# Kernel tuning notes

Hardware: AMD Instinct MI355X
Metric: run time of the kernel (lower is better)

Reference implementation:

```python
import jax, jax.numpy as jnp
import numpy as np

# Conv config (matches init_kwargs)
STRIDE = (1, 1)
PADDING = ((1, 1), (1, 1))
B, CIN, COUT, H, W = 16, 128, 256, 56, 56
KH, KW = 3, 3


def _conv(x, w):
    # NCHW input, OIHW kernel, zeros padding mode
    return jax.lax.conv_general_dilated(
        x, w, window_strides=STRIDE, padding=PADDING,
        dimension_numbers=("NCHW", "OIHW", "NCHW"))


def setup_inputs() -> dict:
    key = jax.random.key(0)
    ks = jax.random.split(key, 6)
    x = jax.random.normal(ks[0], (B, CIN, H, W), dtype=jnp.float32)
    # quantized weight: integer-valued floats (output of module.Q.quantize)
    weight = jnp.round(jax.random.normal(ks[1], (COUT, CIN, KH, KW), dtype=jnp.float32) * 4.0)
    act_s = jnp.asarray(0.0625, dtype=jnp.float32)   # exp2(log_act_s)
    act_q = jnp.asarray(16.0, dtype=jnp.float32)     # exp2(log_act_q)
    azp = jnp.asarray(-4.0, dtype=jnp.float32)       # rounded act zero point (scaled by guard_a)
    wzp = jnp.round(jax.random.normal(ks[2], (COUT,), dtype=jnp.float32) * 2.0)
    fp_scale = (jax.random.uniform(ks[3], (1, COUT, 1, 1), dtype=jnp.float32) + 0.5) * 1e-3
    # bias_full has spatial extent [1, COUT, H_out, W_out]
    bias = jax.random.normal(ks[4], (1, COUT, H, W), dtype=jnp.float32) * 0.1
    guard_a = jnp.asarray(2.0, dtype=jnp.float32)    # 2**act_guard_bit
    guard_w = jnp.asarray(2.0, dtype=jnp.float32)    # 2**weight_guard_bit
    return {"x": x, "weight": weight, "act_s": act_s, "act_q": act_q,
            "azp": azp, "wzp": wzp, "fp_scale": fp_scale, "bias": bias,
            "guard_a": guard_a, "guard_w": guard_w}


def reference(x, weight, act_s, act_q, azp, wzp, fp_scale, bias, guard_a, guard_w):
    # 1) Activation quantization: clamp to quant range then round to integer grid.
    zp = azp * act_s / guard_a
    xq = jnp.clip(x, zp, zp + act_q - act_s)
    xq = guard_a * jnp.round((xq - zp) / act_s)
    # 2) Main integer conv with quantized weights.
    c1 = _conv(xq, weight)
    # 3) Ones-kernel conv: output is identical across all COUT channels,
    #    so compute once as channel-sum followed by a single-channel box conv.
    s = jnp.sum(xq, axis=1, keepdims=True)  # [B, 1, H, W]
    ones_k = jnp.ones((1, 1) + weight.shape[2:], dtype=x.dtype)
    c2 = _conv(s, ones_k)  # [B, 1, H_out, W_out], broadcasts over channels
    # 4) Affine dequant + spatially-varying bias epilogue.
    out = guard_w * c1 + wzp[None, :, None, None] * c2
    return out * fp_scale + bias
```

## Files before the change

kernel.cpp:

```cpp
#include <hip/hip_runtime.h>

#define B_    16
#define CIN_  128
#define COUT_ 256
#define H_    56
#define W_    56
#define YP    58
#define XP    64

typedef int   i32x4 __attribute__((ext_vector_type(4)));
typedef float f4    __attribute__((ext_vector_type(4)));

#define AS_SZ 8192
#define BH_SZ 24704

__device__ __forceinline__ void gload16(const void* g, void* l) {
    __builtin_amdgcn_global_load_lds(
        (const __attribute__((address_space(1))) unsigned int*)g,
        (__attribute__((address_space(3))) unsigned int*)l,
        16, 0, 0);
}

__global__ __launch_bounds__(256) void k_prep(
    const float* __restrict__ x, const float* __restrict__ w,
    const float* __restrict__ p_act_s, const float* __restrict__ p_act_q,
    const float* __restrict__ p_azp,  const float* __restrict__ p_guard_a,
    signed char* __restrict__ xqU, signed char* __restrict__ wt,
    float* __restrict__ s_pad, float* __restrict__ Wsum)
{
    int t = threadIdx.x;
    int blk = blockIdx.x;

    if (blk < 928) {
        int b = blk / YP, y = blk - b * YP;
        __shared__ signed char shq[W_ * 144];
        signed char* orow = xqU + (size_t)blk * XP * CIN_;

        if (y == 0 || y == YP - 1) {
            i32x4 pv = {(int)0x80808080, (int)0x80808080,
                        (int)0x80808080, (int)0x80808080};
            *(i32x4*)(orow + t * 32)      = pv;
            *(i32x4*)(orow + t * 32 + 16) = pv;
            if (t < XP) s_pad[(size_t)blk * XP + t] = 0.0f;
            return;
        }
        int h = y - 1;
        float act_s = p_act_s[0], act_q = p_act_q[0];
        float azp = p_azp[0], ga = p_guard_a[0];
        float zp = azp * act_s / ga;
        float hi = zp + act_q - act_s;
        float inv_s = 1.0f / act_s;

        for (int i = 0; i < 28; ++i) {
            int e = i * 256 + t;
            int cin = e / 56;
            int ww = e - cin * 56;
            float v = x[(((size_t)b * CIN_ + cin) * H_ + h) * W_ + ww];
            v = fminf(fmaxf(v, zp), hi);
            float r = rintf((v - zp) * inv_s);
            float uq = rintf(ga * r * 0.5f) - 128.0f;
            shq[ww * 144 + cin] = (signed char)(int)uq;
        }
        __syncthreads();
        #pragma unroll
        for (int i = 0; i < 2; ++i) {
            int T = i * 256 + t;
            int xx = T >> 3;
            int c16 = T & 7;
            union { i32x4 v; signed char c[16]; } u;
            if (xx >= 1 && xx <= W_) {
                u.v = *(const i32x4*)(shq + (xx - 1) * 144 + c16 * 16);
            } else {
                u.v = (i32x4){(int)0x80808080, (int)0x80808080,
                              (int)0x80808080, (int)0x80808080};
            }
            *(i32x4*)(orow + (size_t)xx * CIN_ + c16 * 16) = u.v;
            int sum = 0;
            #pragma unroll
            for (int j = 0; j < 16; ++j) sum += (int)u.c[j];
            sum += __shfl_xor(sum, 1);
            sum += __shfl_xor(sum, 2);
            sum += __shfl_xor(sum, 4);
            if (c16 == 0)
                s_pad[(size_t)blk * XP + xx] = (float)(2 * sum + 32768);
        }
        return;
    }

    if (blk < 1216) {
        int o = ((blk - 928) * 256 + t) * 4;
        int tile = o >> 13;
        int m    = (o >> 6) & 127;
        int kk   = o & 63;
        int cb = tile & 1, cc = (tile >> 1) & 1, g = tile >> 2;
        int cout = cb * 128 + m;
        int cin0 = cc * 64 + kk;
        int dy = g / 3, dx = g - dy * 3;
        union { int v; signed char c[4]; } pk;
        #pragma unroll
        for (int j = 0; j < 4; ++j) {
            float v = w[(size_t)cout * 1152 + (cin0 + j) * 9 + dy * 3 + dx];
            pk.c[j] = (signed char)(int)v;
        }
        *(int*)(wt + o) = pk.v;
        return;
    }

    {
        int bw = blk - 1216;
        int cout = bw * 16 + (t >> 4);
        int part = t & 15;
        const float* base = w + (size_t)cout * 1152 + part * 72;
        float s = 0.f;
        for (int j = 0; j < 72; ++j) s += base[j];
        s += __shfl_xor(s, 1);
        s += __shfl_xor(s, 2);
        s += __shfl_xor(s, 4);
        s += __shfl_xor(s, 8);
        if (part == 0) Wsum[cout] = s;
        return;
    }
}

__global__ __launch_bounds__(256, 2) void k_gemm(
    const signed char* __restrict__ xqU,
    const signed char* __restrict__ wt,
    const float* __restrict__ s_pad,
    const float* __restrict__ Wsum,
    const float* __restrict__ wzp,
    const float* __restrict__ fps,
    const float* __restrict__ bias,
    const float* __restrict__ p_gw,
    float* __restrict__ out)
{
    __shared__ __align__(16) signed char As[2][AS_SZ];
    __shared__ __align__(16) signed char Bh[2][BH_SZ];
    __shared__ float c2s[4 * 56];

    int tid = threadIdx.x;
    int wv = tid >> 6, lane = tid & 63;
    int xl = lane & 15, q = lane >> 4;
    int p = blockIdx.x, cb = blockIdx.y;
    int b = p / 14, hp = p - b * 14;
    int h = hp * 4;
    int wm0 = (wv >> 1) * 64, wn0 = (wv & 1) * 128;

    if (tid < 224) {
        int rr = tid / 56, wp = tid - rr * 56;
        const float* sp = s_pad + ((size_t)(b * YP + h + rr)) * XP + wp;
        float a = 0.f;
        #pragma unroll
        for (int dy = 0; dy < 3; ++dy)
            #pragma unroll
            for (int dx = 0; dx < 3; ++dx)
                a += sp[dy * XP + dx];
        c2s[tid] = a;
    }

    i32x4 acc[4][8];
    #pragma unroll
    for (int mi = 0; mi < 4; ++mi)
        #pragma unroll
        for (int ni = 0; ni < 8; ++ni)
            acc[mi][ni] = (i32x4){0, 0, 0, 0};

    const signed char* xb = xqU + (size_t)(b * YP + h) * XP * CIN_;

    int a_base = (wm0 + xl) * 64 + q * 16;
    int bn_base[8];
    #pragma unroll
    for (int ni = 0; ni < 8; ++ni) {
        int n = wn0 + ni * 16 + xl;
        int rn = n >> 6, wp = n & 63;
        bn_base[ni] = (rn * XP + wp) * 64 + q * 16;
    }

    #define STAGE_A(buf_, g_, cc_)                                          \
        {                                                                   \
            const signed char* wsrc = wt + (size_t)((((g_)*2+(cc_))*2)+cb) * 8192; \
            signed char* dstb = As[buf_];                                   \
            _Pragma("unroll")                                               \
            for (int r_ = 0; r_ < 2; ++r_)                                  \
                gload16(wsrc + (r_ * 256 + tid) * 16,                       \
                        dstb + (r_ * 256 + wv * 64) * 16);                  \
        }
    #define STAGE_B(buf_, cc_)                                              \
        {                                                                   \
            signed char* dstb = Bh[buf_];                                   \
            _Pragma("unroll")                                               \
            for (int r_ = 0; r_ < 6; ++r_) {                                \
                int T_ = r_ * 256 + tid;                                    \
                int p_ = T_ & 3;                                            \
                int x_ = (T_ >> 2) & 63;                                    \
                int yy_ = T_ >> 8;                                          \
                gload16(xb + (size_t)(yy_ * XP + x_) * CIN_ + (cc_) * 64 + p_ * 16, \
                        dstb + (r_ * 256 + wv * 64) * 16);                  \
            }                                                               \
        }

    STAGE_A(0, 0, 0)
    STAGE_B(0, 0)
    __syncthreads();

    for (int i = 0; i < 18; ++i) {
        int cc = (i >= 9) ? 1 : 0;
        int g = i - cc * 9;
        if (i < 17) {
            int gn = g + 1, ccn = cc;
            if (gn == 9) { gn = 0; ccn = 1; }
            STAGE_A((i + 1) & 1, gn, ccn)
            if (gn == 0) STAGE_B(1, 1)
        }
        {
            const signed char* Ab = As[i & 1];
            const signed char* Bb = Bh[cc];
            int dy = g / 3, dx = g - dy * 3;
            int boff = dy * (XP * 64) + dx * 64;
            i32x4 af[4], bfr[8];
            #pragma unroll
            for (int mi = 0; mi < 4; ++mi)
                af[mi] = *(const i32x4*)(Ab + a_base + mi * 1024);
            #pragma unroll
            for (int ni = 0; ni < 8; ++ni)
                bfr[ni] = *(const i32x4*)(Bb + bn_base[ni] + boff);
            #pragma unroll
            for (int mi = 0; mi < 4; ++mi)
                #pragma unroll
                for (int ni = 0; ni < 8; ++ni)
                    acc[mi][ni] = __builtin_amdgcn_mfma_i32_16x16x64_i8(
                        af[mi], bfr[ni], acc[mi][ni], 0, 0, 0);
        }
        __syncthreads();
    }

    float gw = p_gw[0];
    #pragma unroll
    for (int mi = 0; mi < 4; ++mi) {
        #pragma unroll
        for (int r = 0; r < 4; ++r) {
            int cout = cb * 128 + wm0 + mi * 16 + q * 4 + r;
            float wz = wzp[cout], fs = fps[cout], ws = Wsum[cout];
            #pragma unroll
            for (int ni = 0; ni < 8; ++ni) {
                int n = wn0 + ni * 16 + xl;
                int wp = n & 63;
                if (wp < W_) {
                    int rn = n >> 6;
                    int hrow = h + rn;
                    float c1 = 2.0f * (float)acc[mi][ni][r] + 256.0f * ws;
                    float v = gw * c1 + wz * c2s[rn * 56 + wp];
                    out[(((size_t)b * COUT_ + cout) * H_ + hrow) * W_ + wp] =
                        v * fs + bias[((size_t)cout * H_ + hrow) * W_ + wp];
                }
            }
        }
    }
}

extern "C" void kernel_launch(void* const* d_in, const int* in_sizes, int n_in,
                              void* d_out, int out_size, void* d_ws, size_t ws_size,
                              hipStream_t stream)
{
    const float* x     = (const float*)d_in[0];
    const float* wht   = (const float*)d_in[1];
    const float* act_s = (const float*)d_in[2];
    const float* act_q = (const float*)d_in[3];
    const float* azp   = (const float*)d_in[4];
    const float* wzp   = (const float*)d_in[5];
    const float* fps   = (const float*)d_in[6];
    const float* bias  = (const float*)d_in[7];
    const float* ga    = (const float*)d_in[8];
    const float* gw    = (const float*)d_in[9];
    float* out = (float*)d_out;

    char* ws = (char*)d_ws;
    signed char* xqU  = (signed char*)(ws);
    signed char* wt   = (signed char*)(ws + 7602176);
    float*       spad = (float*)(ws + 7602176 + 294912);
    float*       Wsum = (float*)(ws + 7602176 + 294912 + 237568);

    k_prep<<<dim3(1232), dim3(256), 0, stream>>>(
        x, wht, act_s, act_q, azp, ga, xqU, wt, spad, Wsum);
    k_gemm<<<dim3(224, 2), dim3(256), 0, stream>>>(
        xqU, wt, spad, Wsum, wzp, fps, bias, gw, out);
}
```

Baseline: 143.9 us.

## Halve spatial tile, read weights directly from global, swizzle LDS input layout

Each block now covers 2 output rows instead of 4, so the grid doubles and per-wave accumulators shrink from 4x8 to 4x4 tiles. Weight tiles are no longer staged through LDS with double buffering; each wave loads A fragments straight from global/L2, which removes 16 of the 18 barriers. The input halo tile in LDS is XOR-swizzled across 16-byte slots to cut bank conflicts on B-fragment reads. The trade-off is more redundant halo loads and weight traffic from global memory, in exchange for lower register pressure and higher occupancy.

```diff
diff --git a/kernel.cpp b/kernel.cpp
--- a/kernel.cpp
+++ b/kernel.cpp
@@ -9,10 +9,8 @@
 #define XP    64
 
 typedef int   i32x4 __attribute__((ext_vector_type(4)));
-typedef float f4    __attribute__((ext_vector_type(4)));
-
-#define AS_SZ 8192
-#define BH_SZ 24704
+
+#define BH_SZ 16640
 
 __device__ __forceinline__ void gload16(const void* g, void* l) {
     __builtin_amdgcn_global_load_lds(
@@ -133,19 +131,19 @@
     const float* __restrict__ p_gw,
     float* __restrict__ out)
 {
-    __shared__ __align__(16) signed char As[2][AS_SZ];
     __shared__ __align__(16) signed char Bh[2][BH_SZ];
-    __shared__ float c2s[4 * 56];
+    __shared__ float c2s[2 * 56];
 
     int tid = threadIdx.x;
     int wv = tid >> 6, lane = tid & 63;
     int xl = lane & 15, q = lane >> 4;
     int p = blockIdx.x, cb = blockIdx.y;
-    int b = p / 14, hp = p - b * 14;
-    int h = hp * 4;
-    int wm0 = (wv >> 1) * 64, wn0 = (wv & 1) * 128;
-
-    if (tid < 224) {
+    int b = p / 28, hp = p - b * 28;
+    int h = hp * 2;
+    int wm0 = (wv >> 1) * 64;
+    int row = wv & 1;
+
+    if (tid < 112) {
         int rr = tid / 56, wp = tid - rr * 56;
         const float* sp = s_pad + ((size_t)(b * YP + h + rr)) * XP + wp;
         float a = 0.f;
@@ -157,100 +155,87 @@
         c2s[tid] = a;
     }
 
-    i32x4 acc[4][8];
-    #pragma unroll
-    for (int mi = 0; mi < 4; ++mi)
-        #pragma unroll
-        for (int ni = 0; ni < 8; ++ni)
-            acc[mi][ni] = (i32x4){0, 0, 0, 0};
-
     const signed char* xb = xqU + (size_t)(b * YP + h) * XP * CIN_;
 
-    int a_base = (wm0 + xl) * 64 + q * 16;
-    int bn_base[8];
-    #pragma unroll
-    for (int ni = 0; ni < 8; ++ni) {
-        int n = wn0 + ni * 16 + xl;
-        int rn = n >> 6, wp = n & 63;
-        bn_base[ni] = (rn * XP + wp) * 64 + q * 16;
-    }
-
-    #define STAGE_A(buf_, g_, cc_)                                          \
-        {                                                                   \
-            const signed char* wsrc = wt + (size_t)((((g_)*2+(cc_))*2)+cb) * 8192; \
-            signed char* dstb = As[buf_];                                   \
-            _Pragma("unroll")                                               \
-            for (int r_ = 0; r_ < 2; ++r_)                                  \
-                gload16(wsrc + (r_ * 256 + tid) * 16,                       \
-                        dstb + (r_ * 256 + wv * 64) * 16);                  \
-        }
     #define STAGE_B(buf_, cc_)                                              \
         {                                                                   \
             signed char* dstb = Bh[buf_];                                   \
             _Pragma("unroll")                                               \
-            for (int r_ = 0; r_ < 6; ++r_) {                                \
+            for (int r_ = 0; r_ < 4; ++r_) {                                \
                 int T_ = r_ * 256 + tid;                                    \
                 int p_ = T_ & 3;                                            \
                 int x_ = (T_ >> 2) & 63;                                    \
                 int yy_ = T_ >> 8;                                          \
-                gload16(xb + (size_t)(yy_ * XP + x_) * CIN_ + (cc_) * 64 + p_ * 16, \
+                int q_ = p_ ^ ((x_ >> 1) & 3);                              \
+                gload16(xb + (size_t)(yy_ * XP + x_) * CIN_ + (cc_) * 64 + q_ * 16, \
                         dstb + (r_ * 256 + wv * 64) * 16);                  \
             }                                                               \
         }
 
-    STAGE_A(0, 0, 0)
     STAGE_B(0, 0)
     __syncthreads();
 
-    for (int i = 0; i < 18; ++i) {
-        int cc = (i >= 9) ? 1 : 0;
-        int g = i - cc * 9;
-        if (i < 17) {
-            int gn = g + 1, ccn = cc;
-            if (gn == 9) { gn = 0; ccn = 1; }
-            STAGE_A((i + 1) & 1, gn, ccn)
-            if (gn == 0) STAGE_B(1, 1)
-        }
-        {
-            const signed char* Ab = As[i & 1];
-            const signed char* Bb = Bh[cc];
+    i32x4 acc[4][4];
+    #pragma unroll
+    for (int mi = 0; mi < 4; ++mi)
+        #pragma unroll
+        for (int ni = 0; ni < 4; ++ni)
+            acc[mi][ni] = (i32x4){0, 0, 0, 0};
+
+    int aoff = (wm0 + xl) * 64 + q * 16;
+
+    #pragma unroll
+    for (int cc = 0; cc < 2; ++cc) {
+        const signed char* Bb = Bh[cc];
+        #pragma unroll
+        for (int g = 0; g < 9; ++g) {
+            if (cc == 0 && g == 0) STAGE_B(1, 1)
             int dy = g / 3, dx = g - dy * 3;
-            int boff = dy * (XP * 64) + dx * 64;
-            i32x4 af[4], bfr[8];
+            const signed char* wtile =
+                wt + (size_t)(((g * 2 + cc) * 2) + cb) * 8192;
+            int slot = q ^ (((xl + dx) >> 1) & 3);
+            int boff = (row + dy) * 4096 + (xl + dx) * 64 + slot * 16;
+            i32x4 af[4], bf[4];
             #pragma unroll
             for (int mi = 0; mi < 4; ++mi)
-                af[mi] = *(const i32x4*)(Ab + a_base + mi * 1024);
-            #pragma unroll
-            for (int ni = 0; ni < 8; ++ni)
-                bfr[ni] = *(const i32x4*)(Bb + bn_base[ni] + boff);
+                af[mi] = *(const i32x4*)(wtile + aoff + mi * 1024);
+            #pragma unroll
+            for (int ni = 0; ni < 4; ++ni)
+                bf[ni] = *(const i32x4*)(Bb + boff + ni * 1024);
             #pragma unroll
             for (int mi = 0; mi < 4; ++mi)
                 #pragma unroll
-                for (int ni = 0; ni < 8; ++ni)
+                for (int ni = 0; ni < 4; ++ni)
                     acc[mi][ni] = __builtin_amdgcn_mfma_i32_16x16x64_i8(
-                        af[mi], bfr[ni], acc[mi][ni], 0, 0, 0);
-        }
-        __syncthreads();
-    }
-
+                        af[mi], bf[ni], acc[mi][ni], 0, 0, 0);
+        }
+        if (cc == 0) __syncthreads();
+    }
+
+    int hrow = h + row;
     float gw = p_gw[0];
+    float c2v[4]; int wp4[4];
+    #pragma unroll
+    for (int ni = 0; ni < 4; ++ni) {
+        int wp = ni * 16 + xl;
+        wp4[ni] = wp;
+        c2v[ni] = (wp < W_) ? c2s[row * 56 + wp] : 0.0f;
+    }
     #pragma unroll
     for (int mi = 0; mi < 4; ++mi) {
         #pragma unroll
         for (int r = 0; r < 4; ++r) {
             int cout = cb * 128 + wm0 + mi * 16 + q * 4 + r;
             float wz = wzp[cout], fs = fps[cout], ws = Wsum[cout];
-            #pragma unroll
-            for (int ni = 0; ni < 8; ++ni) {
-                int n = wn0 + ni * 16 + xl;
-                int wp = n & 63;
+            const float* brow = bias + ((size_t)cout * H_ + hrow) * W_;
+            float* orow = out + (((size_t)b * COUT_ + cout) * H_ + hrow) * W_;
+            #pragma unroll
+            for (int ni = 0; ni < 4; ++ni) {
+                int wp = wp4[ni];
                 if (wp < W_) {
-                    int rn = n >> 6;
-                    int hrow = h + rn;
                     float c1 = 2.0f * (float)acc[mi][ni][r] + 256.0f * ws;
-                    float v = gw * c1 + wz * c2s[rn * 56 + wp];
-                    out[(((size_t)b * COUT_ + cout) * H_ + hrow) * W_ + wp] =
-                        v * fs + bias[((size_t)cout * H_ + hrow) * W_ + wp];
+                    float v = gw * c1 + wz * c2v[ni];
+                    orow[wp] = v * fs + brow[wp];
                 }
             }
         }
@@ -281,6 +266,6 @@
 
     k_prep<<<dim3(1232), dim3(256), 0, stream>>>(
         x, wht, act_s, act_q, azp, ga, xqU, wt, spad, Wsum);
-    k_gemm<<<dim3(224, 2), dim3(256), 0, stream>>>(
+    k_gemm<<<dim3(448, 2), dim3(256), 0, stream>>>(
         xqU, wt, spad, Wsum, wzp, fps, bias, gw, out);
 }
```

New measurement: 151.4 us. +5.3%, slower.
